# Performance work log

Measured on AMD Instinct MI355X. Metric: run time of the kernel, lower is better.

The kernel has to match this reference:

```python
import jax, jax.numpy as jnp
import numpy as np


def _lambertw_real(z):
    # Newton iteration for real-branch Lambert W; z is a static python float.
    w = np.log(z) - np.log(np.log(z))
    for _ in range(20):
        ew = np.exp(w)
        w = w - (w * ew - z) / (ew * (w + 1.0))
    return float(w)


def _conv1x1(t, W, b):
    # t: (B,C,H,W), W: (Cout,Cin), b: (Cout,)
    return jnp.einsum('oi,bihw->bohw', W, t) + b[None, :, None, None]


def setup_inputs() -> dict:
    key = jax.random.key(0)
    ks = jax.random.split(key, 6)
    B, C, H, W = 4, 128, 64, 64
    scale = 1.0 / np.sqrt(C)
    return {
        'x': jax.random.normal(ks[0], (B, C, H, W), dtype=jnp.float32),
        'Wq': jax.random.normal(ks[1], (C, C), dtype=jnp.float32) * scale,
        'bq': jax.random.normal(ks[2], (C,), dtype=jnp.float32) * 0.01,
        'Wv': jax.random.normal(ks[3], (C, C), dtype=jnp.float32) * scale,
        'bv': jax.random.normal(ks[4], (C,), dtype=jnp.float32) * 0.01,
        'gamma': jax.random.normal(ks[5], (1,), dtype=jnp.float32) * 0.1,
    }


def reference(x, Wq, bq, Wv, bv, gamma):
    B, C, H, W = x.shape
    N = H * W
    heads = 1

    # Q = 1x1 conv, then (B,C,N) -> permute -> (B,N,C)
    q_img = _conv1x1(x, Wq, bq)
    Q = q_img.reshape(B, C, N).transpose(0, 2, 1)  # (B,N,C)

    # L2-distance scores: ||q_i||^2 + ||q_j||^2 - 2 q_i.q_j, scaled by -1/sqrt(C/heads)
    nq = jnp.sum(Q * Q, axis=2, keepdims=True)  # (B,N,1)
    scores = nq + nq.transpose(0, 2, 1) - 2.0 * jnp.einsum('bnc,bmc->bnm', Q, Q)
    scalar1 = -1.0 / jnp.sqrt(jnp.asarray(C / heads, dtype=jnp.float32))
    P = jax.nn.softmax(scalar1 * scores, axis=-1)  # (B,N,N)

    # NOTE: original uses raw .view(B,N,C) of contiguous (B,C,H,W) -> plain reshape
    attention = jnp.einsum('bnm,bmc->bnc', P, x.reshape(B, N, C))

    A_half = _conv1x1(attention.reshape(B, C, H, W), Wq, bq).reshape(B, N, C)
    scalar2 = 1.0 / jnp.sqrt(jnp.asarray(C, dtype=jnp.float32))
    # bmm(A_half, weight.view(in,out).permute) == A_half @ Wq2d.T for square weight
    attention2 = scalar2 * jnp.einsum('bnk,jk->bnj', A_half, Wq)

    out = _conv1x1(attention2.reshape(B, C, H, W), Wv, bv).reshape(B, N, C)

    # bound = sqrt(N/C) * (4*W(N/e) + 1) * ||Wq||_F * ||Wv||_F
    phi = _lambertw_real(N / np.e)
    bound = jnp.sqrt(jnp.asarray(N / C, dtype=jnp.float32)) * (4.0 * phi + 1.0) \
        * jnp.linalg.norm(Wq) * jnp.linalg.norm(Wv)
    out = out / bound

    out = out.reshape(B, C, H, W)
    return gamma[0] * out + x
```

## Files before the change

kernel.cpp:

```cpp
#include <hip/hip_runtime.h>


typedef __attribute__((ext_vector_type(4))) float f32x4;
typedef __attribute__((ext_vector_type(2))) float f32x2;
typedef __attribute__((ext_vector_type(8))) short s16x8;

#define SCALE_S  0.08838834764831845f
#define SCALE_2S 0.17677669529663689f

__device__ __forceinline__ ushort f2bf(float f){
  uint u = __float_as_uint(f);
  u += 0x7fffu + ((u >> 16) & 1u);
  return (ushort)(u >> 16);
}
__device__ __forceinline__ uint packbf(float lo, float hi){
  return (uint)f2bf(lo) | ((uint)f2bf(hi) << 16);
}

__global__ __launch_bounds__(256) void prep_kernel(const float* __restrict__ Wq, const float* __restrict__ Wv,
                                                   const float* __restrict__ gamma,
                                                   float* __restrict__ WqT, float* __restrict__ WvT,
                                                   float* __restrict__ scale){
  __shared__ float tile[32][33];
  __shared__ float red[256];
  int m = blockIdx.x;
  const float* S = m ? Wv : Wq;
  float* D = m ? WvT : WqT;
  int t = threadIdx.x;
  if (m == 0){
    float sq = 0.f, sv = 0.f;
    for (int i = t*4; i < 16384; i += 1024){
      f32x4 a = *(const f32x4*)(Wq + i);
      f32x4 b = *(const f32x4*)(Wv + i);
      #pragma unroll
      for (int e=0; e<4; e++){ sq += a[e]*a[e]; sv += b[e]*b[e]; }
    }
    red[t] = sq; __syncthreads();
    for (int s = 128; s > 0; s >>= 1){ if (t < s) red[t] += red[t+s]; __syncthreads(); }
    sq = red[0]; __syncthreads();
    red[t] = sv; __syncthreads();
    for (int s = 128; s > 0; s >>= 1){ if (t < s) red[t] += red[t+s]; __syncthreads(); }
    sv = red[0];
    if (t == 0){
      const double PHI = 5.5957572195283385;
      double A = sqrt(32.0) * (4.0*PHI + 1.0);
      float bound = (float)(A * sqrt((double)sq) * sqrt((double)sv));
      scale[0] = gamma[0] / bound;
    }
  }
  int r = t >> 3, cq = (t & 7) * 4;
  for (int tt = 0; tt < 16; tt++){
    int tr = tt >> 2, tc = tt & 3;
    __syncthreads();
    f32x4 v = *(const f32x4*)(S + (tr*32 + r)*128 + tc*32 + cq);
    #pragma unroll
    for (int e=0; e<4; e++) tile[r][cq+e] = v[e];
    __syncthreads();
    f32x4 o;
    #pragma unroll
    for (int e=0; e<4; e++) o[e] = tile[cq+e][r];
    *(f32x4*)(D + (tc*32 + r)*128 + tr*32 + cq) = o;
  }
}

__global__ __launch_bounds__(256) void k1a_qconv(const float* __restrict__ x, const float* __restrict__ WqT,
                                                 const float* __restrict__ bq,
                                                 ushort* __restrict__ Qb, float* __restrict__ biasg){
  __shared__ float nq_part[2][8][2];
  int b = blockIdx.y;
  int n0 = blockIdx.x * 16;
  int c  = threadIdx.x & 127;
  int ng = threadIdx.x >> 7;
  int lane = threadIdx.x & 63;
  int wave = threadIdx.x >> 6;
  const float* xb = x + (size_t)b*524288 + n0 + ng*8;
  float a[8];
  float bias0 = bq[c];
  #pragma unroll
  for (int u=0; u<8; u++) a[u] = bias0;
  for (int i=0; i<128; i++){
    float w = WqT[i*128 + c];
    const float* xr = xb + (size_t)i*4096;
    f32x4 x0 = *(const f32x4*)xr;
    f32x4 x1 = *(const f32x4*)(xr + 4);
    #pragma unroll
    for (int u=0; u<4; u++){
      a[u]   = fmaf(w, x0[u], a[u]);
      a[u+4] = fmaf(w, x1[u], a[u+4]);
    }
  }
  ushort* qb = Qb + (size_t)(b*4096 + n0 + ng*8)*128 + c;
  #pragma unroll
  for (int u=0; u<8; u++) qb[u*128] = f2bf(a[u]);
  #pragma unroll
  for (int u=0; u<8; u++){
    float v = a[u]*a[u];
    #pragma unroll
    for (int d=1; d<64; d<<=1) v += __shfl_xor(v, d, 64);
    if (lane == 0) nq_part[ng][u][wave & 1] = v;
  }
  __syncthreads();
  if (threadIdx.x < 16){
    int g = threadIdx.x >> 3, u = threadIdx.x & 7;
    biasg[b*4096 + n0 + g*8 + u] = SCALE_S * (nq_part[g][u][0] + nq_part[g][u][1]);
  }
}

__global__ __launch_bounds__(256) void k1b_vt(const float* __restrict__ x, ushort* __restrict__ Vt){
  __shared__ __align__(16) ushort t[128*72];
  int b = blockIdx.y; int m0 = blockIdx.x*64;
  const float* xb = x + (size_t)b*524288 + (size_t)m0*128;
  for (int u = threadIdx.x; u < 64*32; u += 256){
    int m = u >> 5, seg = u & 31;
    f32x4 v = *(const f32x4*)(xb + m*128 + seg*4);
    #pragma unroll
    for (int e=0; e<4; e++) t[(seg*4+e)*72 + m] = f2bf(v[e]);
  }
  __syncthreads();
  ushort* vtb = Vt + (size_t)b*524288 + m0;
  for (int u = threadIdx.x; u < 128*8; u += 256){
    int c = u >> 3, seg = u & 7;
    *(s16x8*)(vtb + (size_t)c*4096 + seg*8) = *(const s16x8*)&t[c*72 + seg*8];
  }
}

__global__ __launch_bounds__(256, 2) void k2_flash(const ushort* __restrict__ Qb, const ushort* __restrict__ Vt,
                                                   const float* __restrict__ biasg, float* __restrict__ F0){
  extern __shared__ __align__(16) char smem[];
  int bid = blockIdx.x;
  int xs = bid & 7, jj = bid >> 3;
  int b  = xs >> 1;
  int q0 = ((xs & 1) * 64 + jj) * 32;

  int tid = threadIdx.x;
  int wave = tid >> 6, lane = tid & 63;
  int l15 = lane & 15, l4 = lane >> 4;
  const ushort* Qbb = Qb + (size_t)b*524288;
  const ushort* Vtb = Vt + (size_t)b*524288;
  const float*  bb  = biasg + (size_t)b*4096;
  char* Pb = smem + wave*4096;

  s16x8 qf[2][4];
  #pragma unroll
  for (int qt=0; qt<2; qt++)
    #pragma unroll
    for (int ks=0; ks<4; ks++)
      qf[qt][ks] = *(const s16x8*)(Qbb + (size_t)(q0 + qt*16 + l15)*128 + ks*32 + l4*8);

  f32x4 acc[2][8];
  #pragma unroll
  for (int qt=0; qt<2; qt++)
    #pragma unroll
    for (int ct=0; ct<8; ct++) acc[qt][ct] = (f32x4){0.f,0.f,0.f,0.f};
  float mrun[2] = {-1e30f, -1e30f};
  float lrun[2] = {0.f, 0.f};

  for (int kt=0; kt<16; kt++){
    int m0 = wave*1024 + kt*64;
    f32x4 bv[4];
    #pragma unroll
    for (int mt=0; mt<4; mt++)
      bv[mt] = *(const f32x4*)(bb + m0 + mt*16 + l4*4);

    f32x4 sa[2][4];
    #pragma unroll
    for (int qt=0; qt<2; qt++)
      #pragma unroll
      for (int mt=0; mt<4; mt++) sa[qt][mt] = (f32x4){0.f,0.f,0.f,0.f};
    #pragma unroll
    for (int ks=0; ks<4; ks++){
      s16x8 kb[4];
      #pragma unroll
      for (int mt=0; mt<4; mt++)
        kb[mt] = *(const s16x8*)(Qbb + (size_t)(m0 + mt*16 + l15)*128 + ks*32 + l4*8);
      #pragma unroll
      for (int qt=0; qt<2; qt++)
        #pragma unroll
        for (int mt=0; mt<4; mt++)
          sa[qt][mt] = __builtin_amdgcn_mfma_f32_16x16x32_bf16(kb[mt], qf[qt][ks], sa[qt][mt], 0, 0, 0);
    }
    #pragma unroll
    for (int qt=0; qt<2; qt++){
      #pragma unroll
      for (int mt=0; mt<4; mt++)
        #pragma unroll
        for (int r=0; r<4; r++)
          sa[qt][mt][r] = fmaf(SCALE_2S, sa[qt][mt][r], -bv[mt][r]);
      float m16 = sa[qt][0][0];
      #pragma unroll
      for (int mt=0; mt<4; mt++)
        #pragma unroll
        for (int r=0; r<4; r++) m16 = fmaxf(m16, sa[qt][mt][r]);
      m16 = fmaxf(m16, __shfl_xor(m16, 16, 64));
      m16 = fmaxf(m16, __shfl_xor(m16, 32, 64));
      int need = __any(m16 > mrun[qt]);
      float mn = fmaxf(mrun[qt], m16);
      float corr = 1.0f;
      if (need){ corr = __expf(mrun[qt] - mn); mrun[qt] = mn; }
      float rs = 0.f;
      #pragma unroll
      for (int mt=0; mt<4; mt++)
        #pragma unroll
        for (int r=0; r<4; r++){
          float p = __expf(sa[qt][mt][r] - mn);
          sa[qt][mt][r] = p;
          rs += p;
        }
      rs += __shfl_xor(rs, 16, 64);
      rs += __shfl_xor(rs, 32, 64);
      lrun[qt] = lrun[qt]*corr + rs;
      if (need){
        float cA[4];
        #pragma unroll
        for (int r=0; r<4; r++) cA[r] = __shfl(corr, l4*4 + r, 64);
        #pragma unroll
        for (int ct=0; ct<8; ct++)
          #pragma unroll
          for (int r=0; r<4; r++) acc[qt][ct][r] *= cA[r];
      }
      int row = qt*16 + l15;
      int sw = (row & 7) << 4;
      #pragma unroll
      for (int mt=0; mt<4; mt++){
        uint2 w2;
        w2.x = packbf(sa[qt][mt][0], sa[qt][mt][1]);
        w2.y = packbf(sa[qt][mt][2], sa[qt][mt][3]);
        *(uint2*)(Pb + ((row*128 + mt*32 + l4*8) ^ sw)) = w2;
      }
    }
    int row0 = l15, row1 = 16 + l15;
    int sw0 = (row0 & 7) << 4;
    #pragma unroll
    for (int ks2=0; ks2<2; ks2++){
      s16x8 pa0 = *(const s16x8*)(Pb + ((row0*128 + ks2*64 + l4*16) ^ sw0));
      s16x8 pa1 = *(const s16x8*)(Pb + ((row1*128 + ks2*64 + l4*16) ^ sw0));
      #pragma unroll
      for (int ct=0; ct<8; ct++){
        s16x8 vb = *(const s16x8*)(Vtb + (size_t)(ct*16 + l15)*4096 + m0 + ks2*32 + l4*8);
        acc[0][ct] = __builtin_amdgcn_mfma_f32_16x16x32_bf16(pa0, vb, acc[0][ct], 0, 0, 0);
        acc[1][ct] = __builtin_amdgcn_mfma_f32_16x16x32_bf16(pa1, vb, acc[1][ct], 0, 0, 0);
      }
    }
  }

  float* macc = (float*)smem;
  f32x2* ml   = (f32x2*)(smem + 32768);
  __syncthreads();
  if (wave >= 2){
    int wi = wave - 2;
    #pragma unroll
    for (int qt=0; qt<2; qt++){
      #pragma unroll
      for (int ct=0; ct<8; ct++)
        #pragma unroll
        for (int r=0; r<4; r++)
          macc[wi*4096 + (qt*16 + l4*4 + r)*128 + ct*16 + l15] = acc[qt][ct][r];
      if (lane < 16) ml[wi*32 + qt*16 + lane] = (f32x2){mrun[qt], lrun[qt]};
    }
  }
  __syncthreads();
  float mA[2][4], lA[2][4];
  if (wave < 2){
    int wi = wave;
    #pragma unroll
    for (int qt=0; qt<2; qt++){
      #pragma unroll
      for (int r=0; r<4; r++){
        mA[qt][r] = __shfl(mrun[qt], l4*4 + r, 64);
        lA[qt][r] = __shfl(lrun[qt], l4*4 + r, 64);
        f32x2 pm = ml[wi*32 + qt*16 + l4*4 + r];
        float ms = fmaxf(mA[qt][r], pm.x);
        float aA = __expf(mA[qt][r] - ms);
        float aB = __expf(pm.x - ms);
        lA[qt][r] = aA*lA[qt][r] + aB*pm.y;
        mA[qt][r] = ms;
        #pragma unroll
        for (int ct=0; ct<8; ct++)
          acc[qt][ct][r] = aA*acc[qt][ct][r] + aB*macc[wi*4096 + (qt*16 + l4*4 + r)*128 + ct*16 + l15];
      }
    }
  }
  __syncthreads();
  if (wave == 1){
    #pragma unroll
    for (int qt=0; qt<2; qt++){
      #pragma unroll
      for (int ct=0; ct<8; ct++)
        #pragma unroll
        for (int r=0; r<4; r++)
          macc[(qt*16 + l4*4 + r)*128 + ct*16 + l15] = acc[qt][ct][r];
      if (l15 == 0){
        #pragma unroll
        for (int r=0; r<4; r++)
          ml[qt*16 + l4*4 + r] = (f32x2){mA[qt][r], lA[qt][r]};
      }
    }
  }
  __syncthreads();
  if (wave == 0){
    float* F0b = F0 + (size_t)b*524288;
    #pragma unroll
    for (int qt=0; qt<2; qt++){
      #pragma unroll
      for (int r=0; r<4; r++){
        f32x2 pm = ml[qt*16 + l4*4 + r];
        float ms = fmaxf(mA[qt][r], pm.x);
        float aA = __expf(mA[qt][r] - ms);
        float aB = __expf(pm.x - ms);
        float inv = 1.0f / (aA*lA[qt][r] + aB*pm.y);
        #pragma unroll
        for (int ct=0; ct<8; ct++){
          float ob = macc[(qt*16 + l4*4 + r)*128 + ct*16 + l15];
          F0b[(size_t)(q0 + qt*16 + l4*4 + r)*128 + ct*16 + l15] = (aA*acc[qt][ct][r] + aB*ob) * inv;
        }
      }
    }
  }
}

__global__ __launch_bounds__(256) void g_mid(const float* __restrict__ M, const float* __restrict__ WT,
                                             const float* __restrict__ bias, float* __restrict__ out){
  int b = blockIdx.y;
  int j0 = blockIdx.x * 16;
  int o  = threadIdx.x & 127;
  int jg = threadIdx.x >> 7;
  const float* Mb = M + (size_t)b*524288 + j0 + jg*8;
  float a[8];
  float bo = bias[o];
  #pragma unroll
  for (int u=0; u<8; u++) a[u] = bo;
  for (int i=0; i<128; i++){
    float w = WT[i*128 + o];
    const float* mr = Mb + (size_t)i*4096;
    f32x4 m0 = *(const f32x4*)mr;
    f32x4 m1 = *(const f32x4*)(mr + 4);
    #pragma unroll
    for (int u=0; u<4; u++){
      a[u]   = fmaf(w, m0[u], a[u]);
      a[u+4] = fmaf(w, m1[u], a[u+4]);
    }
  }
  float* ob = out + (size_t)b*524288 + (size_t)o*4096 + j0 + jg*8;
  #pragma unroll
  for (int u=0; u<8; u++) ob[u] = a[u];
}

__global__ __launch_bounds__(256) void g2_bmm(const float* __restrict__ F1, const float* __restrict__ WqT,
                                              float* __restrict__ F2){
  int b = blockIdx.y;
  int n0 = blockIdx.x * 16;
  int p  = threadIdx.x & 127;
  int ng = threadIdx.x >> 7;
  const float* Fb = F1 + (size_t)b*524288 + (size_t)(n0 + ng*8)*128;
  float a[8] = {0.f,0.f,0.f,0.f,0.f,0.f,0.f,0.f};
  for (int k=0; k<128; k++){
    float w = WqT[k*128 + p];
    #pragma unroll
    for (int u=0; u<8; u++) a[u] = fmaf(w, Fb[u*128 + k], a[u]);
  }
  float* ob = F2 + (size_t)b*524288 + (size_t)(n0 + ng*8)*128 + p;
  #pragma unroll
  for (int u=0; u<8; u++) ob[u*128] = a[u] * SCALE_S;
}

__global__ __launch_bounds__(256) void g_final(const float* __restrict__ M, const float* __restrict__ WT,
                                               const float* __restrict__ bias, const float* __restrict__ x,
                                               const float* __restrict__ scale, float* __restrict__ out){
  int b = blockIdx.y;
  int j0 = blockIdx.x * 16;
  int o  = threadIdx.x & 127;
  int jg = threadIdx.x >> 7;
  const float* Mb = M + (size_t)b*524288 + j0 + jg*8;
  float a[8];
  float bo = bias[o];
  #pragma unroll
  for (int u=0; u<8; u++) a[u] = bo;
  for (int i=0; i<128; i++){
    float w = WT[i*128 + o];
    const float* mr = Mb + (size_t)i*4096;
    f32x4 m0 = *(const f32x4*)mr;
    f32x4 m1 = *(const f32x4*)(mr + 4);
    #pragma unroll
    for (int u=0; u<4; u++){
      a[u]   = fmaf(w, m0[u], a[u]);
      a[u+4] = fmaf(w, m1[u], a[u+4]);
    }
  }
  float sc = scale[0];
  const float* xr = x + (size_t)b*524288 + (size_t)o*4096 + j0 + jg*8;
  float* ob = out + (size_t)b*524288 + (size_t)o*4096 + j0 + jg*8;
  #pragma unroll
  for (int u=0; u<8; u++) ob[u] = fmaf(sc, a[u], xr[u]);
}

extern "C" void kernel_launch(void* const* d_in, const int* in_sizes, int n_in,
                              void* d_out, int out_size, void* d_ws, size_t ws_size,
                              hipStream_t stream){
  const float* x     = (const float*)d_in[0];
  const float* Wq    = (const float*)d_in[1];
  const float* bq    = (const float*)d_in[2];
  const float* Wv    = (const float*)d_in[3];
  const float* bv    = (const float*)d_in[4];
  const float* gamma = (const float*)d_in[5];
  char* ws = (char*)d_ws;
  ushort* Qb    = (ushort*)(ws + 0);
  ushort* Vt    = (ushort*)(ws + 4194304);
  float*  F1    = (float*)(ws + 0);
  float*  biasg = (float*)(ws + 8388608);
  float*  WqT   = (float*)(ws + 8454144);
  float*  WvT   = (float*)(ws + 8519680);
  float*  scale = (float*)(ws + 8585216);
  float*  F0    = (float*)(ws + 8585280);
  float*  F2    = F0;
  float*  out   = (float*)d_out;

  prep_kernel<<<2, 256, 0, stream>>>(Wq, Wv, gamma, WqT, WvT, scale);
  k1a_qconv <<<dim3(256,4), 256, 0, stream>>>(x, WqT, bq, Qb, biasg);
  k1b_vt    <<<dim3(64,4),  256, 0, stream>>>(x, Vt);
  k2_flash  <<<512, 256, 33280, stream>>>(Qb, Vt, biasg, F0);
  g_mid     <<<dim3(256,4), 256, 0, stream>>>(F0, WqT, bq, F1);
  g2_bmm    <<<dim3(256,4), 256, 0, stream>>>(F1, WqT, F2);
  g_final   <<<dim3(256,4), 256, 0, stream>>>(F2, WvT, bv, x, scale, out);
}
```

Baseline: 364.1 us.

## Fuse three post-attention 1x1 conv/bmm kernels into one bf16 MFMA kernel

Replaces the three scalar fp32 kernels that followed flash attention (Q conv, Wq bmm, V conv plus residual) with a single kernel. It runs all three products as bf16 MFMA chains through shared memory, working on one image row at a time. The flash kernel now writes bf16 output and handles 16 queries per block instead of 32, launching twice as many blocks, with launch bounds raised to 3. Weights are pre-converted to bf16 in the prep kernel. This removes two fp32 intermediate round trips through global memory and moves the convs onto tensor cores, at the cost of extra bf16 rounding on intermediates and less Q reuse per flash block.

```diff
diff --git a/kernel.cpp b/kernel.cpp
--- a/kernel.cpp
+++ b/kernel.cpp
@@ -19,21 +19,22 @@
 
 __global__ __launch_bounds__(256) void prep_kernel(const float* __restrict__ Wq, const float* __restrict__ Wv,
                                                    const float* __restrict__ gamma,
-                                                   float* __restrict__ WqT, float* __restrict__ WvT,
-                                                   float* __restrict__ scale){
+                                                   float* __restrict__ WqT, ushort* __restrict__ Wqb,
+                                                   ushort* __restrict__ Wvb, float* __restrict__ scale){
   __shared__ float tile[32][33];
   __shared__ float red[256];
-  int m = blockIdx.x;
-  const float* S = m ? Wv : Wq;
-  float* D = m ? WvT : WqT;
   int t = threadIdx.x;
-  if (m == 0){
+  if (blockIdx.x == 0){
     float sq = 0.f, sv = 0.f;
     for (int i = t*4; i < 16384; i += 1024){
       f32x4 a = *(const f32x4*)(Wq + i);
       f32x4 b = *(const f32x4*)(Wv + i);
       #pragma unroll
-      for (int e=0; e<4; e++){ sq += a[e]*a[e]; sv += b[e]*b[e]; }
+      for (int e=0; e<4; e++){
+        sq += a[e]*a[e]; sv += b[e]*b[e];
+        Wqb[i+e] = f2bf(a[e]);
+        Wvb[i+e] = f2bf(b[e]);
+      }
     }
     red[t] = sq; __syncthreads();
     for (int s = 128; s > 0; s >>= 1){ if (t < s) red[t] += red[t+s]; __syncthreads(); }
@@ -47,19 +48,20 @@
       float bound = (float)(A * sqrt((double)sq) * sqrt((double)sv));
       scale[0] = gamma[0] / bound;
     }
-  }
-  int r = t >> 3, cq = (t & 7) * 4;
-  for (int tt = 0; tt < 16; tt++){
-    int tr = tt >> 2, tc = tt & 3;
-    __syncthreads();
-    f32x4 v = *(const f32x4*)(S + (tr*32 + r)*128 + tc*32 + cq);
-    #pragma unroll
-    for (int e=0; e<4; e++) tile[r][cq+e] = v[e];
-    __syncthreads();
-    f32x4 o;
-    #pragma unroll
-    for (int e=0; e<4; e++) o[e] = tile[cq+e][r];
-    *(f32x4*)(D + (tc*32 + r)*128 + tr*32 + cq) = o;
+  } else {
+    int r = t >> 3, cq = (t & 7) * 4;
+    for (int tt = 0; tt < 16; tt++){
+      int tr = tt >> 2, tc = tt & 3;
+      __syncthreads();
+      f32x4 v = *(const f32x4*)(Wq + (tr*32 + r)*128 + tc*32 + cq);
+      #pragma unroll
+      for (int e=0; e<4; e++) tile[r][cq+e] = v[e];
+      __syncthreads();
+      f32x4 o;
+      #pragma unroll
+      for (int e=0; e<4; e++) o[e] = tile[cq+e][r];
+      *(f32x4*)(WqT + (tc*32 + r)*128 + tr*32 + cq) = o;
+    }
   }
 }
 
@@ -124,13 +126,13 @@
   }
 }
 
-__global__ __launch_bounds__(256, 2) void k2_flash(const ushort* __restrict__ Qb, const ushort* __restrict__ Vt,
-                                                   const float* __restrict__ biasg, float* __restrict__ F0){
+__global__ __launch_bounds__(256, 3) void k2_flash(const ushort* __restrict__ Qb, const ushort* __restrict__ Vt,
+                                                   const float* __restrict__ biasg, ushort* __restrict__ F0b16){
   extern __shared__ __align__(16) char smem[];
   int bid = blockIdx.x;
   int xs = bid & 7, jj = bid >> 3;
   int b  = xs >> 1;
-  int q0 = ((xs & 1) * 64 + jj) * 32;
+  int q0 = ((xs & 1) * 128 + jj) * 16;
 
   int tid = threadIdx.x;
   int wave = tid >> 6, lane = tid & 63;
@@ -138,22 +140,19 @@
   const ushort* Qbb = Qb + (size_t)b*524288;
   const ushort* Vtb = Vt + (size_t)b*524288;
   const float*  bb  = biasg + (size_t)b*4096;
-  char* Pb = smem + wave*4096;
-
-  s16x8 qf[2][4];
-  #pragma unroll
-  for (int qt=0; qt<2; qt++)
-    #pragma unroll
-    for (int ks=0; ks<4; ks++)
-      qf[qt][ks] = *(const s16x8*)(Qbb + (size_t)(q0 + qt*16 + l15)*128 + ks*32 + l4*8);
-
-  f32x4 acc[2][8];
-  #pragma unroll
-  for (int qt=0; qt<2; qt++)
-    #pragma unroll
-    for (int ct=0; ct<8; ct++) acc[qt][ct] = (f32x4){0.f,0.f,0.f,0.f};
-  float mrun[2] = {-1e30f, -1e30f};
-  float lrun[2] = {0.f, 0.f};
+  char* Pb = smem + wave*2048;
+
+  s16x8 qf[4];
+  #pragma unroll
+  for (int ks=0; ks<4; ks++)
+    qf[ks] = *(const s16x8*)(Qbb + (size_t)(q0 + l15)*128 + ks*32 + l4*8);
+
+  f32x4 acc[8];
+  #pragma unroll
+  for (int ct=0; ct<8; ct++) acc[ct] = (f32x4){0.f,0.f,0.f,0.f};
+  float mrun = -1e30f, lrun = 0.f;
+
+  int sw = (l15 & 7) << 4;
 
   for (int kt=0; kt<16; kt++){
     int m0 = wave*1024 + kt*64;
@@ -162,11 +161,9 @@
     for (int mt=0; mt<4; mt++)
       bv[mt] = *(const f32x4*)(bb + m0 + mt*16 + l4*4);
 
-    f32x4 sa[2][4];
-    #pragma unroll
-    for (int qt=0; qt<2; qt++)
-      #pragma unroll
-      for (int mt=0; mt<4; mt++) sa[qt][mt] = (f32x4){0.f,0.f,0.f,0.f};
+    f32x4 sa[4];
+    #pragma unroll
+    for (int mt=0; mt<4; mt++) sa[mt] = (f32x4){0.f,0.f,0.f,0.f};
     #pragma unroll
     for (int ks=0; ks<4; ks++){
       s16x8 kb[4];
@@ -174,223 +171,216 @@
       for (int mt=0; mt<4; mt++)
         kb[mt] = *(const s16x8*)(Qbb + (size_t)(m0 + mt*16 + l15)*128 + ks*32 + l4*8);
       #pragma unroll
-      for (int qt=0; qt<2; qt++)
+      for (int mt=0; mt<4; mt++)
+        sa[mt] = __builtin_amdgcn_mfma_f32_16x16x32_bf16(kb[mt], qf[ks], sa[mt], 0, 0, 0);
+    }
+    #pragma unroll
+    for (int mt=0; mt<4; mt++)
+      #pragma unroll
+      for (int r=0; r<4; r++)
+        sa[mt][r] = fmaf(SCALE_2S, sa[mt][r], -bv[mt][r]);
+    float m16 = sa[0][0];
+    #pragma unroll
+    for (int mt=0; mt<4; mt++)
+      #pragma unroll
+      for (int r=0; r<4; r++) m16 = fmaxf(m16, sa[mt][r]);
+    m16 = fmaxf(m16, __shfl_xor(m16, 16, 64));
+    m16 = fmaxf(m16, __shfl_xor(m16, 32, 64));
+    int need = __any(m16 > mrun);
+    float mn = fmaxf(mrun, m16);
+    float corr = 1.0f;
+    if (need){ corr = __expf(mrun - mn); mrun = mn; }
+    float rs = 0.f;
+    #pragma unroll
+    for (int mt=0; mt<4; mt++){
+      #pragma unroll
+      for (int r=0; r<4; r++){
+        float p = __expf(sa[mt][r] - mn);
+        sa[mt][r] = p;
+        rs += p;
+      }
+      uint2 w2;
+      w2.x = packbf(sa[mt][0], sa[mt][1]);
+      w2.y = packbf(sa[mt][2], sa[mt][3]);
+      *(uint2*)(Pb + ((l15*128 + mt*32 + l4*8) ^ sw)) = w2;
+    }
+    rs += __shfl_xor(rs, 16, 64);
+    rs += __shfl_xor(rs, 32, 64);
+    lrun = lrun*corr + rs;
+    if (need){
+      float cA[4];
+      #pragma unroll
+      for (int r=0; r<4; r++) cA[r] = __shfl(corr, l4*4 + r, 64);
+      #pragma unroll
+      for (int ct=0; ct<8; ct++)
         #pragma unroll
-        for (int mt=0; mt<4; mt++)
-          sa[qt][mt] = __builtin_amdgcn_mfma_f32_16x16x32_bf16(kb[mt], qf[qt][ks], sa[qt][mt], 0, 0, 0);
-    }
-    #pragma unroll
-    for (int qt=0; qt<2; qt++){
-      #pragma unroll
-      for (int mt=0; mt<4; mt++)
-        #pragma unroll
-        for (int r=0; r<4; r++)
-          sa[qt][mt][r] = fmaf(SCALE_2S, sa[qt][mt][r], -bv[mt][r]);
-      float m16 = sa[qt][0][0];
-      #pragma unroll
-      for (int mt=0; mt<4; mt++)
-        #pragma unroll
-        for (int r=0; r<4; r++) m16 = fmaxf(m16, sa[qt][mt][r]);
-      m16 = fmaxf(m16, __shfl_xor(m16, 16, 64));
-      m16 = fmaxf(m16, __shfl_xor(m16, 32, 64));
-      int need = __any(m16 > mrun[qt]);
-      float mn = fmaxf(mrun[qt], m16);
-      float corr = 1.0f;
-      if (need){ corr = __expf(mrun[qt] - mn); mrun[qt] = mn; }
-      float rs = 0.f;
-      #pragma unroll
-      for (int mt=0; mt<4; mt++)
-        #pragma unroll
-        for (int r=0; r<4; r++){
-          float p = __expf(sa[qt][mt][r] - mn);
-          sa[qt][mt][r] = p;
-          rs += p;
-        }
-      rs += __shfl_xor(rs, 16, 64);
-      rs += __shfl_xor(rs, 32, 64);
-      lrun[qt] = lrun[qt]*corr + rs;
-      if (need){
-        float cA[4];
-        #pragma unroll
-        for (int r=0; r<4; r++) cA[r] = __shfl(corr, l4*4 + r, 64);
-        #pragma unroll
-        for (int ct=0; ct<8; ct++)
-          #pragma unroll
-          for (int r=0; r<4; r++) acc[qt][ct][r] *= cA[r];
-      }
-      int row = qt*16 + l15;
-      int sw = (row & 7) << 4;
-      #pragma unroll
-      for (int mt=0; mt<4; mt++){
-        uint2 w2;
-        w2.x = packbf(sa[qt][mt][0], sa[qt][mt][1]);
-        w2.y = packbf(sa[qt][mt][2], sa[qt][mt][3]);
-        *(uint2*)(Pb + ((row*128 + mt*32 + l4*8) ^ sw)) = w2;
-      }
-    }
-    int row0 = l15, row1 = 16 + l15;
-    int sw0 = (row0 & 7) << 4;
+        for (int r=0; r<4; r++) acc[ct][r] *= cA[r];
+    }
     #pragma unroll
     for (int ks2=0; ks2<2; ks2++){
-      s16x8 pa0 = *(const s16x8*)(Pb + ((row0*128 + ks2*64 + l4*16) ^ sw0));
-      s16x8 pa1 = *(const s16x8*)(Pb + ((row1*128 + ks2*64 + l4*16) ^ sw0));
+      s16x8 pa = *(const s16x8*)(Pb + ((l15*128 + ks2*64 + l4*16) ^ sw));
       #pragma unroll
       for (int ct=0; ct<8; ct++){
         s16x8 vb = *(const s16x8*)(Vtb + (size_t)(ct*16 + l15)*4096 + m0 + ks2*32 + l4*8);
-        acc[0][ct] = __builtin_amdgcn_mfma_f32_16x16x32_bf16(pa0, vb, acc[0][ct], 0, 0, 0);
-        acc[1][ct] = __builtin_amdgcn_mfma_f32_16x16x32_bf16(pa1, vb, acc[1][ct], 0, 0, 0);
+        acc[ct] = __builtin_amdgcn_mfma_f32_16x16x32_bf16(pa, vb, acc[ct], 0, 0, 0);
       }
     }
   }
 
   float* macc = (float*)smem;
-  f32x2* ml   = (f32x2*)(smem + 32768);
+  f32x2* ml   = (f32x2*)(smem + 16384);
   __syncthreads();
   if (wave >= 2){
     int wi = wave - 2;
     #pragma unroll
-    for (int qt=0; qt<2; qt++){
-      #pragma unroll
-      for (int ct=0; ct<8; ct++)
-        #pragma unroll
-        for (int r=0; r<4; r++)
-          macc[wi*4096 + (qt*16 + l4*4 + r)*128 + ct*16 + l15] = acc[qt][ct][r];
-      if (lane < 16) ml[wi*32 + qt*16 + lane] = (f32x2){mrun[qt], lrun[qt]};
-    }
-  }
-  __syncthreads();
-  float mA[2][4], lA[2][4];
+    for (int ct=0; ct<8; ct++)
+      #pragma unroll
+      for (int r=0; r<4; r++)
+        macc[wi*2048 + (l4*4 + r)*128 + ct*16 + l15] = acc[ct][r];
+    if (lane < 16) ml[wi*16 + lane] = (f32x2){mrun, lrun};
+  }
+  __syncthreads();
+  float mA[4], lA[4];
   if (wave < 2){
     int wi = wave;
     #pragma unroll
-    for (int qt=0; qt<2; qt++){
-      #pragma unroll
-      for (int r=0; r<4; r++){
-        mA[qt][r] = __shfl(mrun[qt], l4*4 + r, 64);
-        lA[qt][r] = __shfl(lrun[qt], l4*4 + r, 64);
-        f32x2 pm = ml[wi*32 + qt*16 + l4*4 + r];
-        float ms = fmaxf(mA[qt][r], pm.x);
-        float aA = __expf(mA[qt][r] - ms);
-        float aB = __expf(pm.x - ms);
-        lA[qt][r] = aA*lA[qt][r] + aB*pm.y;
-        mA[qt][r] = ms;
-        #pragma unroll
-        for (int ct=0; ct<8; ct++)
-          acc[qt][ct][r] = aA*acc[qt][ct][r] + aB*macc[wi*4096 + (qt*16 + l4*4 + r)*128 + ct*16 + l15];
+    for (int r=0; r<4; r++){
+      mA[r] = __shfl(mrun, l4*4 + r, 64);
+      lA[r] = __shfl(lrun, l4*4 + r, 64);
+      f32x2 pm = ml[wi*16 + l4*4 + r];
+      float ms = fmaxf(mA[r], pm.x);
+      float aA = __expf(mA[r] - ms);
+      float aB = __expf(pm.x - ms);
+      lA[r] = aA*lA[r] + aB*pm.y;
+      mA[r] = ms;
+      #pragma unroll
+      for (int ct=0; ct<8; ct++)
+        acc[ct][r] = aA*acc[ct][r] + aB*macc[wi*2048 + (l4*4 + r)*128 + ct*16 + l15];
+    }
+  }
+  __syncthreads();
+  if (wave == 1){
+    #pragma unroll
+    for (int ct=0; ct<8; ct++)
+      #pragma unroll
+      for (int r=0; r<4; r++)
+        macc[(l4*4 + r)*128 + ct*16 + l15] = acc[ct][r];
+    if (l15 == 0){
+      #pragma unroll
+      for (int r=0; r<4; r++)
+        ml[l4*4 + r] = (f32x2){mA[r], lA[r]};
+    }
+  }
+  __syncthreads();
+  if (wave == 0){
+    ushort* Fb = F0b16 + (size_t)b*524288;
+    #pragma unroll
+    for (int r=0; r<4; r++){
+      f32x2 pm = ml[l4*4 + r];
+      float ms = fmaxf(mA[r], pm.x);
+      float aA = __expf(mA[r] - ms);
+      float aB = __expf(pm.x - ms);
+      float inv = 1.0f / (aA*lA[r] + aB*pm.y);
+      #pragma unroll
+      for (int ct=0; ct<8; ct++){
+        float ob = macc[(l4*4 + r)*128 + ct*16 + l15];
+        Fb[(size_t)(q0 + l4*4 + r)*128 + ct*16 + l15] = f2bf((aA*acc[ct][r] + aB*ob) * inv);
       }
     }
   }
-  __syncthreads();
-  if (wave == 1){
-    #pragma unroll
-    for (int qt=0; qt<2; qt++){
-      #pragma unroll
-      for (int ct=0; ct<8; ct++)
-        #pragma unroll
-        for (int r=0; r<4; r++)
-          macc[(qt*16 + l4*4 + r)*128 + ct*16 + l15] = acc[qt][ct][r];
-      if (l15 == 0){
-        #pragma unroll
-        for (int r=0; r<4; r++)
-          ml[qt*16 + l4*4 + r] = (f32x2){mA[qt][r], lA[qt][r]};
-      }
-    }
-  }
-  __syncthreads();
-  if (wave == 0){
-    float* F0b = F0 + (size_t)b*524288;
-    #pragma unroll
-    for (int qt=0; qt<2; qt++){
-      #pragma unroll
-      for (int r=0; r<4; r++){
-        f32x2 pm = ml[qt*16 + l4*4 + r];
-        float ms = fmaxf(mA[qt][r], pm.x);
-        float aA = __expf(mA[qt][r] - ms);
-        float aB = __expf(pm.x - ms);
-        float inv = 1.0f / (aA*lA[qt][r] + aB*pm.y);
-        #pragma unroll
-        for (int ct=0; ct<8; ct++){
-          float ob = macc[(qt*16 + l4*4 + r)*128 + ct*16 + l15];
-          F0b[(size_t)(q0 + qt*16 + l4*4 + r)*128 + ct*16 + l15] = (aA*acc[qt][ct][r] + aB*ob) * inv;
-        }
-      }
-    }
-  }
-}
-
-__global__ __launch_bounds__(256) void g_mid(const float* __restrict__ M, const float* __restrict__ WT,
-                                             const float* __restrict__ bias, float* __restrict__ out){
-  int b = blockIdx.y;
-  int j0 = blockIdx.x * 16;
-  int o  = threadIdx.x & 127;
-  int jg = threadIdx.x >> 7;
-  const float* Mb = M + (size_t)b*524288 + j0 + jg*8;
-  float a[8];
-  float bo = bias[o];
-  #pragma unroll
-  for (int u=0; u<8; u++) a[u] = bo;
-  for (int i=0; i<128; i++){
-    float w = WT[i*128 + o];
-    const float* mr = Mb + (size_t)i*4096;
-    f32x4 m0 = *(const f32x4*)mr;
-    f32x4 m1 = *(const f32x4*)(mr + 4);
-    #pragma unroll
-    for (int u=0; u<4; u++){
-      a[u]   = fmaf(w, m0[u], a[u]);
-      a[u+4] = fmaf(w, m1[u], a[u+4]);
-    }
-  }
-  float* ob = out + (size_t)b*524288 + (size_t)o*4096 + j0 + jg*8;
-  #pragma unroll
-  for (int u=0; u<8; u++) ob[u] = a[u];
-}
-
-__global__ __launch_bounds__(256) void g2_bmm(const float* __restrict__ F1, const float* __restrict__ WqT,
-                                              float* __restrict__ F2){
-  int b = blockIdx.y;
-  int n0 = blockIdx.x * 16;
-  int p  = threadIdx.x & 127;
-  int ng = threadIdx.x >> 7;
-  const float* Fb = F1 + (size_t)b*524288 + (size_t)(n0 + ng*8)*128;
-  float a[8] = {0.f,0.f,0.f,0.f,0.f,0.f,0.f,0.f};
-  for (int k=0; k<128; k++){
-    float w = WqT[k*128 + p];
-    #pragma unroll
-    for (int u=0; u<8; u++) a[u] = fmaf(w, Fb[u*128 + k], a[u]);
-  }
-  float* ob = F2 + (size_t)b*524288 + (size_t)(n0 + ng*8)*128 + p;
-  #pragma unroll
-  for (int u=0; u<8; u++) ob[u*128] = a[u] * SCALE_S;
-}
-
-__global__ __launch_bounds__(256) void g_final(const float* __restrict__ M, const float* __restrict__ WT,
-                                               const float* __restrict__ bias, const float* __restrict__ x,
+}
+
+__global__ __launch_bounds__(512) void g_fused(const ushort* __restrict__ F0b16, const ushort* __restrict__ Wqb,
+                                               const ushort* __restrict__ Wvb, const float* __restrict__ bq,
+                                               const float* __restrict__ bv, const float* __restrict__ x,
                                                const float* __restrict__ scale, float* __restrict__ out){
-  int b = blockIdx.y;
-  int j0 = blockIdx.x * 16;
-  int o  = threadIdx.x & 127;
-  int jg = threadIdx.x >> 7;
-  const float* Mb = M + (size_t)b*524288 + j0 + jg*8;
-  float a[8];
-  float bo = bias[o];
-  #pragma unroll
-  for (int u=0; u<8; u++) a[u] = bo;
-  for (int i=0; i<128; i++){
-    float w = WT[i*128 + o];
-    const float* mr = Mb + (size_t)i*4096;
-    f32x4 m0 = *(const f32x4*)mr;
-    f32x4 m1 = *(const f32x4*)(mr + 4);
-    #pragma unroll
-    for (int u=0; u<4; u++){
-      a[u]   = fmaf(w, m0[u], a[u]);
-      a[u+4] = fmaf(w, m1[u], a[u+4]);
+  extern __shared__ __align__(16) char smem[];
+  ushort* X0T = (ushort*)smem;
+  char*   T1  = smem + 34816;
+  char*   T2  = smem;
+  int bid = blockIdx.x;
+  int xs = bid & 7;
+  int b = xs >> 1;
+  int t = (xs & 1)*16 + (bid >> 3);
+  int tid = threadIdx.x;
+  int wave = tid >> 6, lane = tid & 63;
+  int l15 = lane & 15, l4 = lane >> 4;
+  int m0 = wave * 16;
+  int sw = (l15 & 7) << 4;
+  const ushort* F0bb = F0b16 + (size_t)b*524288;
+
+  {
+    int i = tid >> 2, c4 = (tid & 3) * 32;
+    const ushort* src = F0bb + (size_t)(i*32 + t)*128 + c4;
+    #pragma unroll
+    for (int h=0; h<4; h++){
+      s16x8 v = *(const s16x8*)(src + h*8);
+      #pragma unroll
+      for (int e=0; e<8; e++) X0T[(c4 + h*8 + e)*136 + i] = (ushort)v[e];
+    }
+  }
+  __syncthreads();
+
+  f32x4 acc[8];
+  #pragma unroll
+  for (int nt=0; nt<8; nt++) acc[nt] = (f32x4){0.f,0.f,0.f,0.f};
+  #pragma unroll
+  for (int ks=0; ks<4; ks++){
+    s16x8 af = *(const s16x8*)(X0T + (size_t)(m0 + l15)*136 + ks*32 + l4*8);
+    #pragma unroll
+    for (int nt=0; nt<8; nt++){
+      s16x8 bf = *(const s16x8*)(Wqb + (size_t)(nt*16 + l15)*128 + ks*32 + l4*8);
+      acc[nt] = __builtin_amdgcn_mfma_f32_16x16x32_bf16(af, bf, acc[nt], 0, 0, 0);
+    }
+  }
+  #pragma unroll
+  for (int nt=0; nt<8; nt++){
+    float bqv = bq[nt*16 + l15];
+    uint2 w2;
+    w2.x = packbf(acc[nt][0]+bqv, acc[nt][1]+bqv);
+    w2.y = packbf(acc[nt][2]+bqv, acc[nt][3]+bqv);
+    *(uint2*)(T1 + (((nt*16+l15)*256 + (m0 + l4*4)*2) ^ sw)) = w2;
+  }
+  __syncthreads();
+  #pragma unroll
+  for (int nt=0; nt<8; nt++) acc[nt] = (f32x4){0.f,0.f,0.f,0.f};
+  #pragma unroll
+  for (int ks=0; ks<4; ks++){
+    s16x8 af = *(const s16x8*)(T1 + (((m0 + l15)*256 + ks*64 + l4*16) ^ sw));
+    #pragma unroll
+    for (int nt=0; nt<8; nt++){
+      s16x8 bf = *(const s16x8*)(Wqb + (size_t)(nt*16 + l15)*128 + ks*32 + l4*8);
+      acc[nt] = __builtin_amdgcn_mfma_f32_16x16x32_bf16(af, bf, acc[nt], 0, 0, 0);
+    }
+  }
+  #pragma unroll
+  for (int nt=0; nt<8; nt++){
+    uint2 w2;
+    w2.x = packbf(acc[nt][0]*SCALE_S, acc[nt][1]*SCALE_S);
+    w2.y = packbf(acc[nt][2]*SCALE_S, acc[nt][3]*SCALE_S);
+    *(uint2*)(T2 + (((nt*16+l15)*256 + (m0 + l4*4)*2) ^ sw)) = w2;
+  }
+  __syncthreads();
+  #pragma unroll
+  for (int nt=0; nt<8; nt++) acc[nt] = (f32x4){0.f,0.f,0.f,0.f};
+  #pragma unroll
+  for (int ks=0; ks<4; ks++){
+    s16x8 af = *(const s16x8*)(Wvb + (size_t)(m0 + l15)*128 + ks*32 + l4*8);
+    #pragma unroll
+    for (int nt=0; nt<8; nt++){
+      s16x8 bf = *(const s16x8*)(T2 + (((nt*16+l15)*256 + ks*64 + l4*16) ^ sw));
+      acc[nt] = __builtin_amdgcn_mfma_f32_16x16x32_bf16(af, bf, acc[nt], 0, 0, 0);
     }
   }
   float sc = scale[0];
-  const float* xr = x + (size_t)b*524288 + (size_t)o*4096 + j0 + jg*8;
-  float* ob = out + (size_t)b*524288 + (size_t)o*4096 + j0 + jg*8;
-  #pragma unroll
-  for (int u=0; u<8; u++) ob[u] = fmaf(sc, a[u], xr[u]);
+  f32x4 bvv = *(const f32x4*)(bv + m0 + l4*4);
+  const float* xb = x + (size_t)b*524288 + (size_t)(m0 + l4*4)*4096 + t*128 + l15;
+  float* ob = out + (size_t)b*524288 + (size_t)(m0 + l4*4)*4096 + t*128 + l15;
+  #pragma unroll
+  for (int nt=0; nt<8; nt++)
+    #pragma unroll
+    for (int r=0; r<4; r++)
+      ob[r*4096 + nt*16] = fmaf(sc, acc[nt][r] + bvv[r], xb[r*4096 + nt*16]);
 }
 
 extern "C" void kernel_launch(void* const* d_in, const int* in_sizes, int n_in,
@@ -405,20 +395,17 @@
   char* ws = (char*)d_ws;
   ushort* Qb    = (ushort*)(ws + 0);
   ushort* Vt    = (ushort*)(ws + 4194304);
-  float*  F1    = (float*)(ws + 0);
   float*  biasg = (float*)(ws + 8388608);
   float*  WqT   = (float*)(ws + 8454144);
-  float*  WvT   = (float*)(ws + 8519680);
+  ushort* Wqb   = (ushort*)(ws + 8519680);
+  ushort* Wvb   = (ushort*)(ws + 8552448);
   float*  scale = (float*)(ws + 8585216);
-  float*  F0    = (float*)(ws + 8585280);
-  float*  F2    = F0;
+  ushort* F0b16 = (ushort*)(ws + 8585280);
   float*  out   = (float*)d_out;
 
-  prep_kernel<<<2, 256, 0, stream>>>(Wq, Wv, gamma, WqT, WvT, scale);
+  prep_kernel<<<2, 256, 0, stream>>>(Wq, Wv, gamma, WqT, Wqb, Wvb, scale);
   k1a_qconv <<<dim3(256,4), 256, 0, stream>>>(x, WqT, bq, Qb, biasg);
   k1b_vt    <<<dim3(64,4),  256, 0, stream>>>(x, Vt);
-  k2_flash  <<<512, 256, 33280, stream>>>(Qb, Vt, biasg, F0);
-  g_mid     <<<dim3(256,4), 256, 0, stream>>>(F0, WqT, bq, F1);
-  g2_bmm    <<<dim3(256,4), 256, 0, stream>>>(F1, WqT, F2);
-  g_final   <<<dim3(256,4), 256, 0, stream>>>(F2, WvT, bv, x, scale, out);
-}
+  k2_flash  <<<1024, 256, 16640, stream>>>(Qb, Vt, biasg, F0b16);
+  g_fused   <<<128, 512, 67584, stream>>>(F0b16, Wqb, Wvb, bq, bv, x, scale, out);
+}
```

After: 382.6 us. +5.1%, slower.
